# Optimization experiments

Measured on AMD Instinct MI355X. Metric: run time of the kernel, lower is better.

## Reference

```python
import jax, jax.numpy as jnp
import numpy as np

HIDDEN = 32
N_BLOCKS = 2


def setup_inputs() -> dict:
    key = jax.random.key(0)
    ks = jax.random.split(key, 8)
    B, S, F = 256, 4096, 8
    H = HIDDEN
    inp = {
        "x": jax.random.normal(ks[0], (B, S, F), dtype=jnp.float32),
        # embed
        "W_embed": jax.random.normal(ks[1], (F, H), dtype=jnp.float32) * (F ** -0.5),
        "b_embed": jnp.zeros((H,), jnp.float32),
        # per-block selective-SSM params (stacked over blocks)
        "W_delta": jax.random.normal(ks[2], (N_BLOCKS, H, H), dtype=jnp.float32) * (H ** -0.5),
        "b_delta": jnp.zeros((N_BLOCKS, H), jnp.float32),
        "A_log": jnp.log(jnp.broadcast_to(jnp.arange(1, H + 1, dtype=jnp.float32), (N_BLOCKS, H))),
        "W_gate": jax.random.normal(ks[3], (N_BLOCKS, H, H), dtype=jnp.float32) * (H ** -0.5),
        "b_gate": jnp.zeros((N_BLOCKS, H), jnp.float32),
        # head: LayerNorm + MLP
        "ln_gamma": jnp.ones((H,), jnp.float32),
        "ln_beta": jnp.zeros((H,), jnp.float32),
        "W1": jax.random.normal(ks[4], (H, H), dtype=jnp.float32) * (H ** -0.5),
        "b1": jnp.zeros((H,), jnp.float32),
        "W2": jax.random.normal(ks[5], (H, 1), dtype=jnp.float32) * (H ** -0.5),
        "b2": jnp.zeros((1,), jnp.float32),
    }
    return inp


def _ssm_block(h, Wd, bd, A_log, Wg, bg):
    """Diagonal selective SSM: input-dependent decay, gated output, residual."""
    # h: [B, S, H]
    delta = jax.nn.softplus(jnp.einsum('bsh,hk->bsk', h, Wd) + bd)  # [B,S,H]
    abar = jnp.exp(delta * (-jnp.exp(A_log)))                       # [B,S,H] in (0,1)
    xin = delta * h                                                 # [B,S,H]

    def step(s, ab_xi):
        ab, xi = ab_xi
        s = ab * s + xi
        return s, s

    B, S, H = h.shape
    s0 = jnp.zeros((B, H), h.dtype)
    # scan over time (axis S), vectorized over batch & channels
    _, states = jax.lax.scan(step, s0, (abar.transpose(1, 0, 2), xin.transpose(1, 0, 2)))
    states = states.transpose(1, 0, 2)  # [B,S,H]
    gate = jax.nn.sigmoid(jnp.einsum('bsh,hk->bsk', h, Wg) + bg)
    return h + states * gate


def reference(x, W_embed, b_embed, W_delta, b_delta, A_log, W_gate, b_gate,
              ln_gamma, ln_beta, W1, b1, W2, b2):
    h = jnp.einsum('bsf,fh->bsh', x, W_embed) + b_embed  # [B,S,H]
    for i in range(N_BLOCKS):
        h = _ssm_block(h, W_delta[i], b_delta[i], A_log[i], W_gate[i], b_gate[i])
    hl = h[:, -1, :]  # [B,H] last timestep
    mu = jnp.mean(hl, axis=-1, keepdims=True)
    var = jnp.mean((hl - mu) ** 2, axis=-1, keepdims=True)
    hn = (hl - mu) / jnp.sqrt(var + 1e-5) * ln_gamma + ln_beta
    z = jax.nn.gelu(hn @ W1 + b1)
    return (z @ W2 + b2).squeeze(-1)  # [B]
```

## Files before the change

kernel.cpp:

```cpp
#include <hip/hip_runtime.h>
#include <math.h>

#define BB 256
#define SS 4096
#define FF 8
#define HH 32
#define TT 256
#define NT (SS/TT)
#define NTHREADS 1024
#define NG 16
#define CLR 16

#define L2E  1.4426950408889634f
#define LN2f 0.6931471805599453f

typedef _Float16 f16x8 __attribute__((ext_vector_type(8)));
typedef float    f32x4 __attribute__((ext_vector_type(4)));
typedef __fp16   pk16  __attribute__((ext_vector_type(2)));

__device__ __forceinline__ float fexp2(float x){
#if __has_builtin(__builtin_amdgcn_exp2f)
    return __builtin_amdgcn_exp2f(x);
#else
    return exp2f(x);
#endif
}
__device__ __forceinline__ float flog2(float x){
#if __has_builtin(__builtin_amdgcn_logf)
    return __builtin_amdgcn_logf(x);
#else
    return log2f(x);
#endif
}
__device__ __forceinline__ float frcp(float x){
#if __has_builtin(__builtin_amdgcn_rcpf)
    return __builtin_amdgcn_rcpf(x);
#else
    return 1.0f/x;
#endif
}

__device__ __forceinline__ float softplus_n(float z){
    const float t = fexp2(-fabsf(z) * L2E);
    return fmaxf(z, 0.f) + LN2f * flog2(1.f + t);
}
__device__ __forceinline__ float sigmoid_n(float z){
    return frcp(1.f + fexp2(-z * L2E));
}

__global__ __launch_bounds__(NTHREADS, 4)
void forecast_fused(const float* __restrict__ x,
                    const float* __restrict__ Wemb, const float* __restrict__ bemb,
                    const float* __restrict__ Wd,   const float* __restrict__ bd,
                    const float* __restrict__ Alog,
                    const float* __restrict__ Wg,   const float* __restrict__ bg,
                    const float* __restrict__ gmma, const float* __restrict__ beta,
                    const float* __restrict__ W1,   const float* __restrict__ b1,
                    const float* __restrict__ W2,   const float* __restrict__ b2,
                    float* __restrict__ out)
{
    __shared__ __align__(16) unsigned int xs16[2][TT][4];
    __shared__ __align__(16) unsigned int h1h[TT][16];
    __shared__ float wdpS[FF][HH];
    __shared__ float wgpS[FF][HH];
    __shared__ float bdpS[HH], bgpS[HH];
    __shared__ float2 cfS[2][NG][HH];
    __shared__ float2 cf2S[2][NG][HH];
    __shared__ float s1s[2][HH];
    __shared__ float hlast[HH];

    const int tid  = threadIdx.x;
    const int lane = tid & 63;
    const int g    = tid >> 6;
    const int c0   = lane & 15;
    const int grp  = lane >> 4;
    const int r0   = grp * 4;
    const int cb   = g * CLR;
    const int b    = blockIdx.x;
    const int xrow = tid >> 2, xdc = tid & 3;
    const int lm16 = (lane - 16) & 63, lm32 = (lane - 32) & 63;

    if (tid < FF * HH) {
        const int f = tid >> 5, cc = tid & 31;
        float accd = 0.f, accg = 0.f;
#pragma unroll
        for (int k = 0; k < HH; ++k) {
            const float w = Wemb[f * HH + k];
            accd += w * Wd[k * HH + cc];
            accg += w * Wg[k * HH + cc];
        }
        wdpS[f][cc] = accd;
        wgpS[f][cc] = accg;
    }
    if (tid < HH) {
        float ad = bd[tid], ag = bg[tid];
#pragma unroll
        for (int k = 0; k < HH; ++k) {
            ad += bemb[k] * Wd[k * HH + tid];
            ag += bemb[k] * Wg[k * HH + tid];
        }
        bdpS[tid] = ad; bgpS[tid] = ag;
        s1s[0][tid] = 0.f;
    }
    __syncthreads();

    f16x8 bh0[2], bzd[2], bzg[2], bwd2[2];
    float bec[2], bd1p[2], bg1p[2], bd2c[2], nA1[2], nA2[2];
#pragma unroll
    for (int q = 0; q < 2; ++q) {
        const int cq = c0 + 16 * q;
#pragma unroll
        for (int j = 0; j < 8; ++j) {
            bh0[q][j] = (lane < 16) ? (_Float16)Wemb[j * HH + cq] : (_Float16)0.f;
            bzd[q][j] = (lane < 16) ? (_Float16)wdpS[j][cq]       : (_Float16)0.f;
            bzg[q][j] = (lane < 16) ? (_Float16)wgpS[j][cq]       : (_Float16)0.f;
            bwd2[q][j] = (_Float16)Wd[HH * HH + (grp * 8 + j) * HH + cq];
        }
        bec[q]  = bemb[cq];
        bd1p[q] = bdpS[cq]; bg1p[q] = bgpS[cq];
        bd2c[q] = bd[HH + cq];
        nA1[q] = -expf(Alog[cq]) * L2E;
        nA2[q] = -expf(Alog[HH + cq]) * L2E;
    }

    float s2v = 0.f;

    {
        const float2 xv = *reinterpret_cast<const float2*>(
            x + ((size_t)b * SS + xrow) * FF + xdc * 2);
        const pk16 pk = __builtin_amdgcn_cvt_pkrtz(xv.x, xv.y);
        xs16[0][xrow][xdc] = __builtin_bit_cast(unsigned int, pk);
    }
    __syncthreads();

    for (int it = 0; it < NT; ++it) {
        const int p = it & 1;

        float2 xnext = make_float2(0.f, 0.f);
        if (it + 1 < NT)
            xnext = *reinterpret_cast<const float2*>(
                x + ((size_t)b * SS + (it + 1) * TT + xrow) * FF + xdc * 2);

        uint4 aw = make_uint4(0u, 0u, 0u, 0u);
        if (lane < 16) aw = *reinterpret_cast<const uint4*>(&xs16[p][cb + c0][0]);
        const f16x8 a1 = __builtin_bit_cast(f16x8, aw);
        f32x4 vh0[2], vzd[2], vzg[2];
#pragma unroll
        for (int q = 0; q < 2; ++q) {
            f32x4 cin;
            cin[0] = cin[1] = cin[2] = cin[3] = bec[q];
            vh0[q] = __builtin_amdgcn_mfma_f32_16x16x32_f16(a1, bh0[q], cin, 0, 0, 0);
            cin[0] = cin[1] = cin[2] = cin[3] = bd1p[q];
            vzd[q] = __builtin_amdgcn_mfma_f32_16x16x32_f16(a1, bzd[q], cin, 0, 0, 0);
            cin[0] = cin[1] = cin[2] = cin[3] = bg1p[q];
            vzg[q] = __builtin_amdgcn_mfma_f32_16x16x32_f16(a1, bzg[q], cin, 0, 0, 0);
        }

        float pA[2][4], pl[2][4], gt[2][4], h1v[2][4];
#pragma unroll
        for (int q = 0; q < 2; ++q) {
            float sp = 1.f, sl = 0.f;
#pragma unroll
            for (int j = 0; j < 4; ++j) {
                const float delta = softplus_n(vzd[q][j]);
                const float ab    = fexp2(delta * nA1[q]);
                sl = ab * sl + delta * vh0[q][j];
                sp *= ab;
                pA[q][j] = sp; pl[q][j] = sl;
                gt[q][j] = sigmoid_n(vzg[q][j]);
            }
        }
        float P[2], S[2];
        P[0] = pA[0][3]; S[0] = pl[0][3];
        P[1] = pA[1][3]; S[1] = pl[1][3];
#pragma unroll
        for (int q = 0; q < 2; ++q) {
            float Pm = __shfl(P[q], lm16), Sm = __shfl(S[q], lm16);
            if (grp >= 1) { S[q] = P[q] * Sm + S[q]; P[q] = P[q] * Pm; }
            float Pm2 = __shfl(P[q], lm32), Sm2 = __shfl(S[q], lm32);
            if (grp >= 2) { S[q] = P[q] * Sm2 + S[q]; P[q] = P[q] * Pm2; }
        }
        if (grp == 3) {
            cfS[p][g][c0]      = make_float2(P[0], S[0]);
            cfS[p][g][c0 + 16] = make_float2(P[1], S[1]);
        }
        __syncthreads();

        const int chc = lane & 31;
        float cy = s1s[p][chc];
#pragma unroll
        for (int ch = 0; ch < NG; ++ch) {
            const float2 ax = cfS[p][ch][chc];
            const float t = ax.x * cy + ax.y;
            cy = (ch < g) ? t : cy;
        }
        if (g == NG - 1 && lane < 32) {
            const float2 aL = cfS[p][NG - 1][chc];
            s1s[p ^ 1][chc] = aL.x * cy + aL.y;
        }
        const float cyq0 = __shfl(cy, c0);
        const float cyq1 = __shfl(cy, c0 + 16);
        float gin[2];
#pragma unroll
        for (int q = 0; q < 2; ++q) {
            float Pe = __shfl(P[q], lm16), Se = __shfl(S[q], lm16);
            if (grp == 0) { Pe = 1.f; Se = 0.f; }
            gin[q] = Se + Pe * (q ? cyq1 : cyq0);
        }

#pragma unroll
        for (int q = 0; q < 2; ++q)
#pragma unroll
            for (int j = 0; j < 4; ++j) {
                const float st = pl[q][j] + pA[q][j] * gin[q];
                h1v[q][j] = vh0[q][j] + st * gt[q][j];
            }
#pragma unroll
        for (int j = 0; j < 4; ++j) {
            const float p0 = __shfl_xor(h1v[0][j], 1);
            const float p1 = __shfl_xor(h1v[1][j], 1);
            unsigned int w;
            if (lane & 1) {
                const pk16 pk = __builtin_amdgcn_cvt_pkrtz(p1, h1v[1][j]);
                w = __builtin_bit_cast(unsigned int, pk);
            } else {
                const pk16 pk = __builtin_amdgcn_cvt_pkrtz(h1v[0][j], p0);
                w = __builtin_bit_cast(unsigned int, pk);
            }
            h1h[cb + r0 + j][(c0 >> 1) + ((lane & 1) ? 8 : 0)] = w;
        }
        if (it == NT - 1 && g == NG - 1 && grp == 3) {
            hlast[c0]      = h1v[0][3];
            hlast[c0 + 16] = h1v[1][3];
        }

        const uint4 aw2 = *reinterpret_cast<const uint4*>(&h1h[cb + c0][grp * 4]);
        const f16x8 a2 = __builtin_bit_cast(f16x8, aw2);
        float P2[2], S2[2];
#pragma unroll
        for (int q = 0; q < 2; ++q) {
            f32x4 cin;
            cin[0] = cin[1] = cin[2] = cin[3] = bd2c[q];
            const f32x4 vd2 = __builtin_amdgcn_mfma_f32_16x16x32_f16(a2, bwd2[q], cin, 0, 0, 0);
            float sp = 1.f, sl = 0.f;
#pragma unroll
            for (int j = 0; j < 4; ++j) {
                const float delta = softplus_n(vd2[j]);
                const float ab    = fexp2(delta * nA2[q]);
                sl = ab * sl + delta * h1v[q][j];
                sp *= ab;
            }
            P2[q] = sp; S2[q] = sl;
        }
#pragma unroll
        for (int q = 0; q < 2; ++q) {
            float Pm = __shfl(P2[q], lm16), Sm = __shfl(S2[q], lm16);
            if (grp >= 1) { S2[q] = P2[q] * Sm + S2[q]; P2[q] = P2[q] * Pm; }
            float Pm2 = __shfl(P2[q], lm32), Sm2 = __shfl(S2[q], lm32);
            if (grp >= 2) { S2[q] = P2[q] * Sm2 + S2[q]; P2[q] = P2[q] * Pm2; }
        }
        if (grp == 3) {
            cf2S[p][g][c0]      = make_float2(P2[0], S2[0]);
            cf2S[p][g][c0 + 16] = make_float2(P2[1], S2[1]);
        }
        if (it + 1 < NT) {
            const pk16 pk = __builtin_amdgcn_cvt_pkrtz(xnext.x, xnext.y);
            xs16[p ^ 1][xrow][xdc] = __builtin_bit_cast(unsigned int, pk);
        }
        __syncthreads();

        if (tid < 32) {
            float cy2 = s2v;
#pragma unroll
            for (int ch = 0; ch < NG; ++ch) {
                const float2 ax = cf2S[p][ch][tid];
                cy2 = ax.x * cy2 + ax.y;
            }
            s2v = cy2;
        }
    }
    __syncthreads();

    if (tid < HH) {
        float zg = bg[HH + tid];
#pragma unroll
        for (int k = 0; k < HH; ++k) zg += hlast[k] * Wg[HH * HH + k * HH + tid];
        const float gt2 = sigmoid_n(zg);
        const float h2  = hlast[tid] + s2v * gt2;

        float sum = h2;
#pragma unroll
        for (int m = 1; m < HH; m <<= 1) sum += __shfl_xor(sum, m);
        const float mu = sum * (1.0f / HH);
        const float d  = h2 - mu;
        float vs = d * d;
#pragma unroll
        for (int m = 1; m < HH; m <<= 1) vs += __shfl_xor(vs, m);
        const float rstd = rsqrtf(vs * (1.0f / HH) + 1e-5f);
        const float hn   = d * rstd * gmma[tid] + beta[tid];

        float z = b1[tid];
#pragma unroll
        for (int k = 0; k < HH; ++k) z += __shfl(hn, k) * W1[k * HH + tid];
        const float u  = 2.0f * L2E * 0.7978845608028654f * (z + 0.044715f * z * z * z);
        const float e  = fexp2(u);
        const float th = 1.f - 2.f * frcp(1.f + e);
        const float ge = 0.5f * z * (1.0f + th);
        float v = ge * W2[tid];
#pragma unroll
        for (int m = 1; m < HH; m <<= 1) v += __shfl_xor(v, m);
        if (tid == 0) out[b] = v + b2[0];
    }
}

extern "C" void kernel_launch(void* const* d_in, const int* in_sizes, int n_in,
                              void* d_out, int out_size, void* d_ws, size_t ws_size,
                              hipStream_t stream) {
    const float* x    = (const float*)d_in[0];
    const float* Wemb = (const float*)d_in[1];
    const float* bemb = (const float*)d_in[2];
    const float* Wd   = (const float*)d_in[3];
    const float* bd   = (const float*)d_in[4];
    const float* Alog = (const float*)d_in[5];
    const float* Wg   = (const float*)d_in[6];
    const float* bg   = (const float*)d_in[7];
    const float* gmma = (const float*)d_in[8];
    const float* beta = (const float*)d_in[9];
    const float* W1   = (const float*)d_in[10];
    const float* b1   = (const float*)d_in[11];
    const float* W2   = (const float*)d_in[12];
    const float* b2   = (const float*)d_in[13];
    float* out = (float*)d_out;

    forecast_fused<<<dim3(BB), dim3(NTHREADS), 0, stream>>>(
        x, Wemb, bemb, Wd, bd, Alog, Wg, bg, gmma, beta, W1, b1, W2, b2, out);
}
```

Measured before the change: 167.0 us.

## Drop per-chunk block barrier via wave-local x staging and deferred carry

```diff
diff --git a/kernel.cpp b/kernel.cpp
--- a/kernel.cpp
+++ b/kernel.cpp
@@ -10,6 +10,7 @@
 #define NTHREADS 1024
 #define NG 16
 #define CLR 16
+#define HROW 20
 
 #define L2E  1.4426950408889634f
 #define LN2f 0.6931471805599453f
@@ -48,7 +49,7 @@
     return frcp(1.f + fexp2(-z * L2E));
 }
 
-__global__ __launch_bounds__(NTHREADS, 4)
+__global__ __launch_bounds__(NTHREADS)
 void forecast_fused(const float* __restrict__ x,
                     const float* __restrict__ Wemb, const float* __restrict__ bemb,
                     const float* __restrict__ Wd,   const float* __restrict__ bd,
@@ -59,8 +60,8 @@
                     const float* __restrict__ W2,   const float* __restrict__ b2,
                     float* __restrict__ out)
 {
-    __shared__ __align__(16) unsigned int xs16[2][TT][4];
-    __shared__ __align__(16) unsigned int h1h[TT][16];
+    __shared__ __align__(16) unsigned int xs16[TT][4];
+    __shared__ __align__(16) unsigned int h1h[TT][HROW];
     __shared__ float wdpS[FF][HH];
     __shared__ float wgpS[FF][HH];
     __shared__ float bdpS[HH], bgpS[HH];
@@ -77,8 +78,9 @@
     const int r0   = grp * 4;
     const int cb   = g * CLR;
     const int b    = blockIdx.x;
-    const int xrow = tid >> 2, xdc = tid & 3;
     const int lm16 = (lane - 16) & 63, lm32 = (lane - 32) & 63;
+    const int srow = cb + (lane >> 2);
+    const int sdc  = lane & 3;
 
     if (tid < FF * HH) {
         const int f = tid >> 5, cc = tid & 31;
@@ -127,11 +129,10 @@
 
     {
         const float2 xv = *reinterpret_cast<const float2*>(
-            x + ((size_t)b * SS + xrow) * FF + xdc * 2);
+            x + ((size_t)b * SS + srow) * FF + sdc * 2);
         const pk16 pk = __builtin_amdgcn_cvt_pkrtz(xv.x, xv.y);
-        xs16[0][xrow][xdc] = __builtin_bit_cast(unsigned int, pk);
-    }
-    __syncthreads();
+        xs16[srow][sdc] = __builtin_bit_cast(unsigned int, pk);
+    }
 
     for (int it = 0; it < NT; ++it) {
         const int p = it & 1;
@@ -139,10 +140,10 @@
         float2 xnext = make_float2(0.f, 0.f);
         if (it + 1 < NT)
             xnext = *reinterpret_cast<const float2*>(
-                x + ((size_t)b * SS + (it + 1) * TT + xrow) * FF + xdc * 2);
+                x + ((size_t)b * SS + (it + 1) * TT + srow) * FF + sdc * 2);
 
         uint4 aw = make_uint4(0u, 0u, 0u, 0u);
-        if (lane < 16) aw = *reinterpret_cast<const uint4*>(&xs16[p][cb + c0][0]);
+        if (lane < 16) aw = *reinterpret_cast<const uint4*>(&xs16[cb + c0][0]);
         const f16x8 a1 = __builtin_bit_cast(f16x8, aw);
         f32x4 vh0[2], vzd[2], vzg[2];
 #pragma unroll
@@ -263,25 +264,34 @@
             cf2S[p][g][c0]      = make_float2(P2[0], S2[0]);
             cf2S[p][g][c0 + 16] = make_float2(P2[1], S2[1]);
         }
+
+        if (it > 0 && tid < 32) {
+            float cy2 = s2v;
+#pragma unroll
+            for (int ch = 0; ch < NG; ++ch) {
+                const float2 ax = cf2S[p ^ 1][ch][tid];
+                cy2 = ax.x * cy2 + ax.y;
+            }
+            s2v = cy2;
+        }
+
         if (it + 1 < NT) {
             const pk16 pk = __builtin_amdgcn_cvt_pkrtz(xnext.x, xnext.y);
-            xs16[p ^ 1][xrow][xdc] = __builtin_bit_cast(unsigned int, pk);
-        }
-        __syncthreads();
-
-        if (tid < 32) {
+            xs16[srow][sdc] = __builtin_bit_cast(unsigned int, pk);
+        }
+    }
+    __syncthreads();
+
+    if (tid < HH) {
+        {
             float cy2 = s2v;
 #pragma unroll
             for (int ch = 0; ch < NG; ++ch) {
-                const float2 ax = cf2S[p][ch][tid];
+                const float2 ax = cf2S[(NT - 1) & 1][ch][tid];
                 cy2 = ax.x * cy2 + ax.y;
             }
             s2v = cy2;
         }
-    }
-    __syncthreads();
-
-    if (tid < HH) {
         float zg = bg[HH + tid];
 #pragma unroll
         for (int k = 0; k < HH; ++k) zg += hlast[k] * Wg[HH * HH + k * HH + tid];
```

Result: no change. 163.8 us (-1.9%).
